# Performance work log

Hardware: AMD Instinct MI355X
Metric: run time of the kernel (lower is better)

Reference implementation:

```python
import jax, jax.numpy as jnp
import numpy as np

N_QUBITS = 12
N_LAYERS = 3
HID = 16
IN_DIM = 6
BATCH = 4096
C64 = jnp.complex64


def _ry(t):
    c = jnp.cos(t / 2).astype(C64)
    s = jnp.sin(t / 2).astype(C64)
    return jnp.stack([jnp.stack([c, -s], -1), jnp.stack([s, c], -1)], -2)


def _rx(t):
    c = jnp.cos(t / 2).astype(C64)
    s = jnp.sin(t / 2).astype(C64)
    js = 1j * s
    return jnp.stack([jnp.stack([c, -js], -1), jnp.stack([-js, c], -1)], -2)


def _rz(t):
    e = jnp.exp(-1j * t.astype(C64) / 2)
    z = jnp.zeros_like(e)
    return jnp.stack([jnp.stack([e, z], -1), jnp.stack([z, jnp.conj(e)], -1)], -2)


def _apply_1q(state, U, wire):
    # state: (B,) + (2,)*n ; U: (2,2) shared or (B,2,2) per-sample
    s = jnp.moveaxis(state, wire + 1, 1)
    if U.ndim == 2:
        s = jnp.einsum('ij,bj...->bi...', U, s)
    else:
        s = jnp.einsum('bij,bj...->bi...', U, s)
    return jnp.moveaxis(s, 1, wire + 1)


def _cnot(state, c, t):
    ax_c = c + 1
    s0 = jnp.take(state, 0, axis=ax_c)
    s1 = jnp.take(state, 1, axis=ax_c)
    t_ax = t + 1 if t < c else t  # target axis after removing control axis
    s1 = jnp.flip(s1, axis=t_ax)  # X on target when control=1
    return jnp.stack([s0, s1], axis=ax_c)


def _quantum(angles, qparams):
    # angles: (B, n_qubits) angle-encoding RY rotations; qparams: (L, n, 3)
    B = angles.shape[0]
    n = N_QUBITS
    state = jnp.zeros((B,) + (2,) * n, C64).at[(slice(None),) + (0,) * n].set(1.0)
    for i in range(n):
        state = _apply_1q(state, _ry(angles[:, i]), i)
    for l in range(N_LAYERS):
        for i in range(n):
            # RX then RY then RZ on wire i -> fused 2x2
            U = _rz(qparams[l, i, 2]) @ _ry(qparams[l, i, 1]) @ _rx(qparams[l, i, 0])
            state = _apply_1q(state, U, i)
        for i in range(n - 1):
            state = _cnot(state, i, i + 1)
        if n > 2:
            state = _cnot(state, n - 1, 0)
    p = state.real ** 2 + state.imag ** 2  # (B,) + (2,)*n
    evs = []
    for i in range(n):
        axes = tuple(a for a in range(1, n + 1) if a != i + 1)
        pi = p.sum(axes)  # (B, 2)
        evs.append(pi[:, 0] - pi[:, 1])
    return jnp.stack(evs, axis=1)  # (B, n) PauliZ expvals


def setup_inputs() -> dict:
    key = jax.random.key(0)
    ks = jax.random.split(key, 14)
    w = lambda k, shape: jax.random.normal(k, shape, jnp.float32) * 0.1
    return {
        'x': jax.random.normal(ks[0], (BATCH, IN_DIM), jnp.float32),
        'W1': w(ks[1], (HID, IN_DIM)), 'b1': w(ks[2], (HID,)),
        'W2': w(ks[3], (HID, HID)), 'b2': w(ks[4], (HID,)),
        'W3': w(ks[5], (N_QUBITS, HID)), 'b3': w(ks[6], (N_QUBITS,)),
        'qparams': w(ks[7], (N_LAYERS, N_QUBITS, 3)),
        'P1': w(ks[8], (HID, N_QUBITS)), 'c1': w(ks[9], (HID,)),
        'P2': w(ks[10], (8, HID)), 'c2': w(ks[11], (8,)),
        'P3': w(ks[12], (1, 8)), 'c3': w(ks[13], (1,)),
    }


def reference(x, W1, b1, W2, b2, W3, b3, qparams, P1, c1, P2, c2, P3, c3):
    # classical preprocessor (dropout = identity at inference)
    h = jax.nn.relu(x @ W1.T + b1)
    h = jax.nn.relu(h @ W2.T + b2)
    angles = h @ W3.T + b3  # (B, n_qubits)
    q = _quantum(angles, qparams)  # (B, n_qubits)
    # classical postprocessor
    o = jax.nn.relu(q @ P1.T + c1)
    o = jax.nn.relu(o @ P2.T + c2)
    o = jax.nn.sigmoid(o @ P3.T + c3)
    return o.squeeze(-1)  # (B,)
```

## Files before the change

kernel.cpp:

```cpp
#include <hip/hip_runtime.h>
#include <stdint.h>

#define NQ   12
#define DIM  4096
#define TPB  256

typedef float   v2f   __attribute__((ext_vector_type(2)));
typedef float   v4f   __attribute__((ext_vector_type(4)));
typedef float   f32x4 __attribute__((ext_vector_type(4)));
typedef _Float16 v2h  __attribute__((ext_vector_type(2)));
typedef _Float16 f16x8 __attribute__((ext_vector_type(8)));
typedef uint32_t u32x4 __attribute__((ext_vector_type(4)));

struct PassL {
  uint32_t v[4], m[4];
  uint32_t Be[8];
  uint8_t  np[8];
  uint8_t  layer, wb;
};
struct PassC {
  uint16_t WD[8];
  uint16_t WQ1, WQ2;
  uint16_t WV0, WV3;
  uint16_t SM[12];
  uint8_t  robin[12];
  uint8_t  layer, wb;
};
struct InitC { uint16_t ICt[8]; uint16_t ICj[16]; };

constexpr int par(uint32_t x) { return __builtin_popcount(x) & 1; }

constexpr void bmm(uint32_t* C, const uint32_t* A, const uint32_t* B) {
  for (int i = 0; i < NQ; ++i) {
    uint32_t r = 0;
    for (int j = 0; j < NQ; ++j) if ((A[i] >> j) & 1u) r ^= B[j];
    C[i] = r;
  }
}
constexpr void binv(const uint32_t* M, uint32_t* Inv) {
  uint32_t A[NQ] = {}, I[NQ] = {};
  for (int i = 0; i < NQ; ++i) { A[i] = M[i]; I[i] = 1u << i; }
  for (int c = 0; c < NQ; ++c) {
    int piv = -1;
    for (int r = c; r < NQ; ++r) if ((A[r] >> c) & 1u) { piv = r; break; }
    if (piv < 0) continue;
    uint32_t ta = A[c]; A[c] = A[piv]; A[piv] = ta;
    uint32_t ti = I[c]; I[c] = I[piv]; I[piv] = ti;
    for (int r = 0; r < NQ; ++r)
      if (r != c && ((A[r] >> c) & 1u)) { A[r] ^= A[c]; I[r] ^= I[c]; }
  }
  for (int i = 0; i < NQ; ++i) Inv[i] = I[i];
}
constexpr int rank5(const uint32_t* cols, int n) {
  uint32_t rows[5] = {}; int rnk = 0;
  for (int q = 0; q < n; ++q) {
    uint32_t x = cols[q] & 31u;
    for (int bit = 4; bit >= 0; --bit) {
      if (!((x >> bit) & 1u)) continue;
      if (rows[bit]) { x ^= rows[bit]; }
      else { rows[bit] = x; ++rnk; break; }
    }
  }
  return rnk;
}

constexpr PassL passL_default(int p) {
  PassL L{};
  uint32_t A[NQ] = {}; A[0] = 0xFFEu;
  for (int i = 1; i < NQ; ++i) A[i] = (1u << (i + 1)) - 1u;
  uint32_t A2[NQ] = {}, Ai[NQ] = {}, A2i[NQ] = {};
  bmm(A2, A, A); binv(A, Ai); binv(A2, A2i);
  const int Lr = (p < 3) ? 1 : 2, wb = (p % 3) * 4;
  const uint32_t* M  = (Lr == 1) ? A  : A2;
  const uint32_t* Mi = (Lr == 1) ? Ai : A2i;
  for (int i = 0; i < 4; ++i) {
    const int w = wb + i; uint32_t col = 0;
    for (int r = 0; r < NQ; ++r) col |= ((Mi[r] >> w) & 1u) << r;
    L.v[i] = col; L.m[i] = M[w];
  }
  uint32_t Bc[NQ] = {};
  for (int b = 0; b < NQ; ++b) {
    uint32_t col = 1u << b;
    for (int i = 0; i < 4; ++i) if ((L.m[i] >> b) & 1u) col ^= L.v[i];
    Bc[b] = col;
  }
  uint32_t redv[4] = {}; uint32_t pivmask = 0;
  for (int i = 0; i < 4; ++i) {
    redv[i] = L.v[i];
    for (int k = 0; k < i; ++k) {
      int pb = 0;
      for (int b = 0; b < NQ; ++b) if ((redv[k] >> b) & 1u) pb = b;
      if ((redv[i] >> pb) & 1u) redv[i] ^= redv[k];
    }
    int pb = 0;
    for (int b = 0; b < NQ; ++b) if ((redv[i] >> b) & 1u) pb = b;
    pivmask |= 1u << pb;
  }
  int c = 0;
  for (int b = 0; b < NQ; ++b)
    if (!((pivmask >> b) & 1u)) { L.np[c] = (uint8_t)b; L.Be[c] = Bc[b]; ++c; }
  L.layer = (uint8_t)Lr; L.wb = (uint8_t)wb;
  return L;
}

constexpr uint8_t ASSIGN[12] = {0, 1, 6, 7, 2, 3, 4, 5, 8, 9, 10, 11};
struct Lam { uint32_t minv[NQ]; };
constexpr Lam make_lam(const PassL& L) {
  uint32_t bas[12] = {L.v[0], L.v[1], L.v[2], L.v[3],
                      L.Be[0], L.Be[1], L.Be[2], L.Be[3],
                      L.Be[4], L.Be[5], L.Be[6], L.Be[7]};
  uint32_t Mr[NQ] = {};
  for (int i = 0; i < NQ; ++i) {
    uint32_t r = 0;
    for (int j = 0; j < NQ; ++j) r |= ((bas[j] >> i) & 1u) << j;
    Mr[i] = r;
  }
  Lam lm{};
  binv(Mr, lm.minv);
  return lm;
}
constexpr uint32_t lap(const Lam& lm, uint32_t y) {
  uint32_t r = 0;
  for (int j = 0; j < NQ; ++j)
    if (par(lm.minv[j] & y)) r ^= 1u << ASSIGN[j];
  return r;
}

constexpr int P4[24][4] = {
  {0,1,2,3},{0,1,3,2},{0,2,1,3},{0,2,3,1},{0,3,1,2},{0,3,2,1},
  {1,0,2,3},{1,0,3,2},{1,2,0,3},{1,2,3,0},{1,3,0,2},{1,3,2,0},
  {2,0,1,3},{2,0,3,1},{2,1,0,3},{2,1,3,0},{2,3,0,1},{2,3,1,0},
  {3,0,1,2},{3,0,2,1},{3,1,0,2},{3,1,2,0},{3,2,0,1},{3,2,1,0}};

constexpr PassL reorder_np(const PassL& L, int pi, int s45, int s67) {
  PassL T = L;
  for (int k = 0; k < 4; ++k) { T.np[k] = L.np[P4[pi][k]]; T.Be[k] = L.Be[P4[pi][k]]; }
  if (s45) { T.np[4] = L.np[5]; T.np[5] = L.np[4]; T.Be[4] = L.Be[5]; T.Be[5] = L.Be[4]; }
  if (s67) { T.np[6] = L.np[7]; T.np[7] = L.np[6]; T.Be[6] = L.Be[7]; T.Be[7] = L.Be[6]; }
  return T;
}

constexpr PassL passL_ordered(int p, const PassL& prev) {
  const PassL L = passL_default(p);
  int best = -1; PassL bestL = L;
  for (int pi = 0; pi < 24; ++pi)
  for (int s45 = 0; s45 < 2; ++s45)
  for (int s67 = 0; s67 < 2; ++s67) {
    const PassL T = reorder_np(L, pi, s45, s67);
    const Lam lm = make_lam(T);
    uint32_t g[8] = { lap(lm, prev.Be[0]), lap(lm, prev.Be[1]),
                      lap(lm, prev.Be[2]), lap(lm, prev.Be[3]),
                      lap(lm, prev.v[1]),  lap(lm, prev.v[2]),
                      lap(lm, prev.Be[6]), lap(lm, prev.Be[7]) };
    const int r = rank5(g, 8);
    if (r > best) { best = r; bestL = T; }
  }
  return bestL;
}

constexpr PassL L0 = passL_default(0);
constexpr PassL L1 = passL_ordered(1, L0);
constexpr PassL L2 = passL_ordered(2, L1);
constexpr PassL L3 = passL_ordered(3, L2);
constexpr PassL L4 = passL_ordered(4, L3);
constexpr PassL L5 = passL_ordered(5, L4);

constexpr PassC make_passC(const PassL& L, const PassL& Ln) {
  PassC c{};
  const Lam lm = make_lam(Ln);
  for (int k = 0; k < 8; ++k) c.WD[k] = (uint16_t)lap(lm, L.Be[k]);
  c.WQ1 = (uint16_t)lap(lm, L.v[1]); c.WQ2 = (uint16_t)lap(lm, L.v[2]);
  c.WV0 = (uint16_t)lap(lm, L.v[0]); c.WV3 = (uint16_t)lap(lm, L.v[3]);
  c.layer = L.layer; c.wb = L.wb;
  return c;
}
constexpr PassC make_passC5(const PassL& L) {
  PassC c{};
  uint32_t A[NQ] = {}; A[0] = 0xFFEu;
  for (int i = 1; i < NQ; ++i) A[i] = (1u << (i + 1)) - 1u;
  uint32_t A2[NQ] = {}, A3[NQ] = {};
  bmm(A2, A, A); bmm(A3, A2, A);
  for (int i = 0; i < NQ; ++i) {
    uint32_t sm = 0;
    sm |= (uint32_t)par(A3[i] & L.Be[0]) << 0;
    sm |= (uint32_t)par(A3[i] & L.Be[1]) << 1;
    sm |= (uint32_t)par(A3[i] & L.Be[2]) << 2;
    sm |= (uint32_t)par(A3[i] & L.Be[3]) << 3;
    sm |= (uint32_t)par(A3[i] & L.v[1])  << 4;
    sm |= (uint32_t)par(A3[i] & L.v[2])  << 5;
    sm |= (uint32_t)par(A3[i] & L.Be[6]) << 6;
    sm |= (uint32_t)par(A3[i] & L.Be[7]) << 7;
    c.SM[i] = (uint16_t)sm;
    uint32_t b = (uint32_t)par(A3[i] & L.v[0])
               | (uint32_t)par(A3[i] & L.v[3])  << 1
               | (uint32_t)par(A3[i] & L.Be[4]) << 2
               | (uint32_t)par(A3[i] & L.Be[5]) << 3;
    c.robin[i] = (uint8_t)b;
  }
  c.layer = L.layer; c.wb = L.wb;
  return c;
}
constexpr InitC make_init(const PassL& L) {
  InitC ic{};
  const Lam lm = make_lam(L);
  for (int b = 0; b < 8; ++b) ic.ICt[b] = (uint16_t)lap(lm, 1u << b);
  uint32_t Jc[4] = {};
  for (int b = 0; b < 4; ++b) Jc[b] = lap(lm, 1u << (8 + b));
  for (int j = 0; j < 16; ++j) {
    uint32_t r = 0;
    for (int b = 0; b < 4; ++b) if ((j >> b) & 1) r ^= Jc[b];
    ic.ICj[j] = (uint16_t)r;
  }
  return ic;
}

constexpr PassC C0 = make_passC(L0, L1);
constexpr PassC C1 = make_passC(L1, L2);
constexpr PassC C2 = make_passC(L2, L3);
constexpr PassC C3 = make_passC(L3, L4);
constexpr PassC C4 = make_passC(L4, L5);
constexpr PassC C5 = make_passC5(L5);
constexpr InitC IC = make_init(L0);

template<int P> constexpr PassC cget() {
  if constexpr (P == 0) return C0;
  else if constexpr (P == 1) return C1;
  else if constexpr (P == 2) return C2;
  else if constexpr (P == 3) return C3;
  else if constexpr (P == 4) return C4;
  else return C5;
}

__device__ __forceinline__ v2f cmulf(v2f a, v2f b) {
  return (v2f){a.x * b.x - a.y * b.y, a.x * b.y + a.y * b.x};
}
__device__ __forceinline__ uint32_t f2h2(float a, float b) {
  return __builtin_bit_cast(uint32_t, __builtin_amdgcn_cvt_pkrtz(a, b));
}
__device__ __forceinline__ uint32_t pk_rtn(float a, float b) {
  v2h h = {(_Float16)a, (_Float16)b};
  return __builtin_bit_cast(uint32_t, h);
}
__device__ __forceinline__ void build_u(const float* __restrict__ qp, int l, int w, float U[8]) {
  float p0 = qp[(l * 12 + w) * 3 + 0];
  float p1 = qp[(l * 12 + w) * 3 + 1];
  float p2 = qp[(l * 12 + w) * 3 + 2];
  float cx, sx, cy, sy, cz, sz;
  sincosf(0.5f * p0, &sx, &cx);
  sincosf(0.5f * p1, &sy, &cy);
  sincosf(0.5f * p2, &sz, &cz);
  float M00x =  cy * cx, M00y =  sy * sx;
  float M01x = -sy * cx, M01y = -cy * sx;
  float M10x =  sy * cx, M10y = -cy * sx;
  float M11x =  cy * cx, M11y = -sy * sx;
  U[0] = cz * M00x + sz * M00y; U[1] = cz * M00y - sz * M00x;
  U[2] = cz * M01x + sz * M01y; U[3] = cz * M01y - sz * M01x;
  U[4] = cz * M10x - sz * M10y; U[5] = cz * M10y + sz * M10x;
  U[6] = cz * M11x - sz * M11y; U[7] = cz * M11y + sz * M11x;
}
__device__ __forceinline__ int am_col(int c, int i) {
  return ((((c >> 2) ^ ((i >> 1) & 3)) << 2) | (c & 3));
}

template<int P>
__device__ __forceinline__ void build_am_g(uint32_t* __restrict__ Am_g,
                                           const v2f (*gg)[12][4], int t) {
  constexpr PassC pc = cget<P>();
  const int r_ = t >> 4, c_ = t & 15;
  v2f e = (v2f){1.f, 0.f};
  #pragma unroll
  for (int i = 0; i < 4; ++i) {
    v2f u = gg[pc.layer - 1][pc.wb + i][(((r_ >> i) & 1) << 1) | ((c_ >> i) & 1)];
    e = cmulf(e, u);
  }
  const int ra = 2 * r_, rb = 2 * r_ + 1;
  Am_g[P * 512 + ra * 16 + am_col(c_, ra)] = pk_rtn(e.x, -e.y);
  Am_g[P * 512 + rb * 16 + am_col(c_, rb)] = pk_rtn(e.y, e.x);
}

__global__ __launch_bounds__(256) void prep_kernel(const float* __restrict__ qp,
                                                   uint32_t* __restrict__ Am_g,
                                                   float* __restrict__ U0_g) {
  __shared__ v2f gg[2][12][4];
  const int t = threadIdx.x;
  if (t < 24) {
    const int L = t / 12 + 1, w = t % 12;
    float U[8]; build_u(qp, L, w, U);
    gg[L - 1][w][0] = (v2f){U[0], U[1]};
    gg[L - 1][w][1] = (v2f){U[2], U[3]};
    gg[L - 1][w][2] = (v2f){U[4], U[5]};
    gg[L - 1][w][3] = (v2f){U[6], U[7]};
  } else if (t >= 32 && t < 44) {
    const int w = t - 32;
    float U[8]; build_u(qp, 0, w, U);
    #pragma unroll
    for (int k = 0; k < 8; ++k) U0_g[w * 8 + k] = U[k];
  }
  __syncthreads();
  build_am_g<0>(Am_g, gg, t);
  build_am_g<1>(Am_g, gg, t);
  build_am_g<2>(Am_g, gg, t);
  build_am_g<3>(Am_g, gg, t);
  build_am_g<4>(Am_g, gg, t);
  build_am_g<5>(Am_g, gg, t);
}

template<int P, bool LAST>
__device__ __forceinline__ void do_pass(uint32_t* st, f16x8 a0, f16x8 a1,
                                        int t, float* ev) {
  constexpr PassC pc = cget<P>();
  const int lane = t & 63, wv = t >> 6;
  const int n = lane & 15, q = lane >> 4;
  const int rb = (n << 2) | (q << 6) | (wv << 10);
  int wb_ = 0;
  if constexpr (!LAST) {
    wb_ = ((n & 1) ? pc.WD[0] : 0) ^ ((n & 2) ? pc.WD[1] : 0)
        ^ ((n & 4) ? pc.WD[2] : 0) ^ ((n & 8) ? pc.WD[3] : 0)
        ^ ((q & 1) ? pc.WQ1 : 0)   ^ ((q & 2) ? pc.WQ2 : 0)
        ^ ((wv & 1) ? pc.WD[6] : 0) ^ ((wv & 2) ? pc.WD[7] : 0);
  }
  float pr[16];
  const f32x4 z = {0.f, 0.f, 0.f, 0.f};
  #pragma unroll
  for (int T = 0; T < 4; ++T) {
    u32x4 braw = *reinterpret_cast<const u32x4*>(&st[rb + (T << 8)]);
    f16x8 bf = __builtin_bit_cast(f16x8, braw);
    f32x4 c0 = __builtin_amdgcn_mfma_f32_16x16x32_f16(a0, bf, z, 0, 0, 0);
    f32x4 c1 = __builtin_amdgcn_mfma_f32_16x16x32_f16(a1, bf, z, 0, 0, 0);
    if constexpr (!LAST) {
      const int wa = wb_ ^ ((T & 1) ? pc.WD[4] : 0) ^ ((T & 2) ? pc.WD[5] : 0);
      st[wa]                       = f2h2(c0.x, c0.y);
      st[wa ^ pc.WV0]              = f2h2(c0.z, c0.w);
      st[wa ^ pc.WV3]              = f2h2(c1.x, c1.y);
      st[wa ^ (pc.WV0 ^ pc.WV3)]   = f2h2(c1.z, c1.w);
    } else {
      const int nb = ((T & 1) << 2) | ((T >> 1) << 3);
      pr[nb]     = c0.x * c0.x + c0.y * c0.y;
      pr[nb | 1] = c0.z * c0.z + c0.w * c0.w;
      pr[nb | 2] = c1.x * c1.x + c1.y * c1.y;
      pr[nb | 3] = c1.z * c1.z + c1.w * c1.w;
    }
  }
  if constexpr (LAST) {
    #pragma unroll
    for (int gs = 1; gs < 16; gs <<= 1) {
      #pragma unroll
      for (int j = 0; j < 16; ++j) {
        if (j & gs) continue;
        float u = pr[j], w2 = pr[j | gs];
        pr[j] = u + w2; pr[j | gs] = u - w2;
      }
    }
    const int pw = n | (q << 4) | (wv << 6);
    #pragma unroll
    for (int i = 0; i < NQ; ++i) {
      float h = pr[pc.robin[i]];
      int s = (__popc(pc.SM[i] & pw) & 1) << 31;
      ev[i] = __int_as_float(__float_as_int(h) ^ s);
    }
  }
}

#define LDA(P, A0, A1) {                                                        \
  const int li_ = lane & 15;                                                    \
  const int q_  = (lane >> 4) ^ ((li_ >> 1) & 3);                               \
  A0 = __builtin_bit_cast(f16x8,                                                \
      *reinterpret_cast<const u32x4*>(Am_g + (P) * 512 + li_ * 16 + q_ * 4));   \
  A1 = __builtin_bit_cast(f16x8,                                                \
      *reinterpret_cast<const u32x4*>(Am_g + (P) * 512 + (li_ + 16) * 16 + q_ * 4)); \
}

__global__ __launch_bounds__(TPB, 8) void hqc_kernel(
    const float* __restrict__ x,  const float* __restrict__ W1, const float* __restrict__ b1,
    const float* __restrict__ W2, const float* __restrict__ b2,
    const float* __restrict__ W3, const float* __restrict__ b3,
    const float* __restrict__ P1, const float* __restrict__ c1,
    const float* __restrict__ P2, const float* __restrict__ c2,
    const float* __restrict__ P3, const float* __restrict__ c3,
    const uint32_t* __restrict__ Am_g, const float* __restrict__ U0_g,
    float* __restrict__ out)
{
  __shared__ __align__(16) uint32_t st[DIM];
  __shared__ v4f  gpk0[12][2];
  __shared__ float red[4][NQ];

  const int s    = blockIdx.x;
  const int t    = threadIdx.x;
  const int lane = t & 63;
  const int wv   = t >> 6;

  f16x8 a0c, a1c, a0n, a1n;
  LDA(0, a0c, a1c)

  if (wv == 0 && lane < 16) {
    float a = b1[lane];
    #pragma unroll
    for (int k = 0; k < 6; ++k) a = fmaf(W1[lane * 6 + k], x[s * 6 + k], a);
    float h1 = fmaxf(a, 0.f);
    float a2 = b2[lane];
    #pragma unroll
    for (int k = 0; k < 16; ++k) a2 = fmaf(W2[lane * 16 + k], __shfl(h1, k, 64), a2);
    float h2 = fmaxf(a2, 0.f);
    const int lw = (lane < NQ) ? lane : 0;
    float a3 = b3[lw];
    #pragma unroll
    for (int k = 0; k < 16; ++k) a3 = fmaf(W3[lw * 16 + k], __shfl(h2, k, 64), a3);
    if (lane < NQ) {
      const float* u = U0_g + lane * 8;
      float ca, sa; sincosf(0.5f * a3, &sa, &ca);
      float c0x = u[0] * ca + u[2] * sa, c0y = u[1] * ca + u[3] * sa;
      float c1x = u[4] * ca + u[6] * sa, c1y = u[5] * ca + u[7] * sa;
      gpk0[lane][0] = (v4f){c0x, c0x, -c0y, c0y};
      gpk0[lane][1] = (v4f){c1x, c1x, -c1y, c1y};
    }
  }
  __syncthreads();

  {
    int tb = 0;
    #pragma unroll
    for (int b = 0; b < 8; ++b) if ((t >> b) & 1) tb ^= IC.ICt[b];
    v2f acc = (v2f){1.f, 0.f};
    #pragma unroll
    for (int i = 0; i < 8; ++i) {
      v4f gk = gpk0[i][(t >> i) & 1];
      acc = gk.xy * acc + gk.zw * acc.yx;
    }
    v2f l16[16];
    l16[0] = acc;
    #pragma unroll
    for (int i = 0; i < 4; ++i) {
      v4f g0 = gpk0[8 + i][0], g1 = gpk0[8 + i][1];
      #pragma unroll
      for (int j = 0; j < (1 << i); ++j) {
        v2f a = l16[j];
        l16[j | (1 << i)] = g1.xy * a + g1.zw * a.yx;
        l16[j]            = g0.xy * a + g0.zw * a.yx;
      }
    }
    #pragma unroll
    for (int j = 0; j < 16; ++j) st[tb ^ IC.ICj[j]] = f2h2(l16[j].x, l16[j].y);
  }
  __syncthreads();

  float ev[NQ];
  LDA(1, a0n, a1n)
  do_pass<0, false>(st, a0c, a1c, t, ev); __syncthreads();
  a0c = a0n; a1c = a1n; LDA(2, a0n, a1n)
  do_pass<1, false>(st, a0c, a1c, t, ev); __syncthreads();
  a0c = a0n; a1c = a1n; LDA(3, a0n, a1n)
  do_pass<2, false>(st, a0c, a1c, t, ev); __syncthreads();
  a0c = a0n; a1c = a1n; LDA(4, a0n, a1n)
  do_pass<3, false>(st, a0c, a1c, t, ev); __syncthreads();
  a0c = a0n; a1c = a1n; LDA(5, a0n, a1n)
  do_pass<4, false>(st, a0c, a1c, t, ev); __syncthreads();
  a0c = a0n; a1c = a1n;
  do_pass<5, true >(st, a0c, a1c, t, ev);

  #pragma unroll
  for (int off = 32; off >= 1; off >>= 1) {
    #pragma unroll
    for (int i = 0; i < NQ; ++i) ev[i] += __shfl_xor(ev[i], off, 64);
  }
  if (lane == 0) {
    #pragma unroll
    for (int i = 0; i < NQ; ++i) red[wv][i] = ev[i];
  }
  __syncthreads();

  if (wv == 0 && lane < 16) {
    float q = (lane < NQ)
      ? (red[0][lane] + red[1][lane] + red[2][lane] + red[3][lane])
      : 0.f;
    float a = c1[lane];
    #pragma unroll
    for (int j = 0; j < NQ; ++j) a = fmaf(P1[lane * NQ + j], __shfl(q, j, 64), a);
    float o1 = fmaxf(a, 0.f);
    float a2 = c2[lane & 7];
    #pragma unroll
    for (int j = 0; j < 16; ++j) a2 = fmaf(P2[(lane & 7) * 16 + j], __shfl(o1, j, 64), a2);
    float o2 = fmaxf(a2, 0.f);
    float a3 = c3[0];
    #pragma unroll
    for (int j = 0; j < 8; ++j) a3 = fmaf(P3[j], __shfl(o2, j, 64), a3);
    if (lane == 0) out[s] = 1.f / (1.f + expf(-a3));
  }
}

extern "C" void kernel_launch(void* const* d_in, const int* in_sizes, int n_in,
                              void* d_out, int out_size, void* d_ws, size_t ws_size,
                              hipStream_t stream) {
  (void)in_sizes; (void)n_in; (void)ws_size;
  uint32_t* Am_g = (uint32_t*)d_ws;
  float*    U0_g = (float*)((char*)d_ws + 6 * 512 * 4);
  const float* qp = (const float*)d_in[7];
  prep_kernel<<<1, 256, 0, stream>>>(qp, Am_g, U0_g);
  hqc_kernel<<<out_size, TPB, 0, stream>>>(
      (const float*)d_in[0],  (const float*)d_in[1],  (const float*)d_in[2],
      (const float*)d_in[3],  (const float*)d_in[4],  (const float*)d_in[5],
      (const float*)d_in[6],
      (const float*)d_in[8],  (const float*)d_in[9],
      (const float*)d_in[10], (const float*)d_in[11],
      (const float*)d_in[12], (const float*)d_in[13],
      Am_g, U0_g,
      (float*)d_out);
}
```

Measured before the change: 48.28 us.

## Rebuild GF(2) state basis with XOR-swizzled LDS addressing to avoid bank conflicts

Replaces the permutation-search basis selection with a new construction that picks basis vectors from neighbouring passes and solves for XOR signature corrections (G matrices). LDS read and write addresses are swizzled with these signatures so MFMA B-operand loads and fp16 writebacks land on distinct banks. When the write pattern allows it, the code emits paired adjacent stores with select-based swaps instead of four scattered stores. The cost is extra XOR address math per lane and considerably more complex compile-time construction, with some risk that the swizzle is wrong.

```diff
diff --git a/kernel.cpp b/kernel.cpp
--- a/kernel.cpp
+++ b/kernel.cpp
@@ -12,23 +12,9 @@
 typedef _Float16 f16x8 __attribute__((ext_vector_type(8)));
 typedef uint32_t u32x4 __attribute__((ext_vector_type(4)));
 
-struct PassL {
-  uint32_t v[4], m[4];
-  uint32_t Be[8];
-  uint8_t  np[8];
-  uint8_t  layer, wb;
-};
-struct PassC {
-  uint16_t WD[8];
-  uint16_t WQ1, WQ2;
-  uint16_t WV0, WV3;
-  uint16_t SM[12];
-  uint8_t  robin[12];
-  uint8_t  layer, wb;
-};
-struct InitC { uint16_t ICt[8]; uint16_t ICj[16]; };
 
 constexpr int par(uint32_t x) { return __builtin_popcount(x) & 1; }
+constexpr int chbit(uint32_t x) { int b=-1; for (int i=0;i<32;++i) if ((x>>i)&1u) b=i; return b; }
 
 constexpr void bmm(uint32_t* C, const uint32_t* A, const uint32_t* B) {
   for (int i = 0; i < NQ; ++i) {
@@ -51,185 +37,216 @@
   }
   for (int i = 0; i < NQ; ++i) Inv[i] = I[i];
 }
-constexpr int rank5(const uint32_t* cols, int n) {
-  uint32_t rows[5] = {}; int rnk = 0;
-  for (int q = 0; q < n; ++q) {
-    uint32_t x = cols[q] & 31u;
-    for (int bit = 4; bit >= 0; --bit) {
-      if (!((x >> bit) & 1u)) continue;
-      if (rows[bit]) { x ^= rows[bit]; }
-      else { rows[bit] = x; ++rnk; break; }
-    }
-  }
-  return rnk;
-}
-
-constexpr PassL passL_default(int p) {
-  PassL L{};
+
+constexpr void pass_v(int p, uint32_t* v) {
   uint32_t A[NQ] = {}; A[0] = 0xFFEu;
   for (int i = 1; i < NQ; ++i) A[i] = (1u << (i + 1)) - 1u;
   uint32_t A2[NQ] = {}, Ai[NQ] = {}, A2i[NQ] = {};
   bmm(A2, A, A); binv(A, Ai); binv(A2, A2i);
-  const int Lr = (p < 3) ? 1 : 2, wb = (p % 3) * 4;
-  const uint32_t* M  = (Lr == 1) ? A  : A2;
-  const uint32_t* Mi = (Lr == 1) ? Ai : A2i;
+  const uint32_t* Mi = (p < 3) ? Ai : A2i;
+  const int wb = (p % 3) * 4;
   for (int i = 0; i < 4; ++i) {
-    const int w = wb + i; uint32_t col = 0;
-    for (int r = 0; r < NQ; ++r) col |= ((Mi[r] >> w) & 1u) << r;
-    L.v[i] = col; L.m[i] = M[w];
-  }
-  uint32_t Bc[NQ] = {};
-  for (int b = 0; b < NQ; ++b) {
-    uint32_t col = 1u << b;
-    for (int i = 0; i < 4; ++i) if ((L.m[i] >> b) & 1u) col ^= L.v[i];
-    Bc[b] = col;
-  }
-  uint32_t redv[4] = {}; uint32_t pivmask = 0;
-  for (int i = 0; i < 4; ++i) {
-    redv[i] = L.v[i];
-    for (int k = 0; k < i; ++k) {
-      int pb = 0;
-      for (int b = 0; b < NQ; ++b) if ((redv[k] >> b) & 1u) pb = b;
-      if ((redv[i] >> pb) & 1u) redv[i] ^= redv[k];
-    }
-    int pb = 0;
-    for (int b = 0; b < NQ; ++b) if ((redv[i] >> b) & 1u) pb = b;
-    pivmask |= 1u << pb;
-  }
-  int c = 0;
-  for (int b = 0; b < NQ; ++b)
-    if (!((pivmask >> b) & 1u)) { L.np[c] = (uint8_t)b; L.Be[c] = Bc[b]; ++c; }
-  L.layer = (uint8_t)Lr; L.wb = (uint8_t)wb;
-  return L;
-}
-
-constexpr uint8_t ASSIGN[12] = {0, 1, 6, 7, 2, 3, 4, 5, 8, 9, 10, 11};
-struct Lam { uint32_t minv[NQ]; };
-constexpr Lam make_lam(const PassL& L) {
-  uint32_t bas[12] = {L.v[0], L.v[1], L.v[2], L.v[3],
-                      L.Be[0], L.Be[1], L.Be[2], L.Be[3],
-                      L.Be[4], L.Be[5], L.Be[6], L.Be[7]};
+    uint32_t col = 0;
+    for (int r = 0; r < NQ; ++r) col |= ((Mi[r] >> (wb + i)) & 1u) << r;
+    v[i] = col;
+  }
+}
+
+constexpr bool addvec(uint32_t* red, uint32_t x) {
+  while (x) {
+    const int h = chbit(x);
+    if (red[h]) x ^= red[h]; else { red[h] = x; return true; }
+  }
+  return false;
+}
+constexpr bool tryindep(const uint32_t* red, uint32_t x) {
+  uint32_t tmp[16] = {};
+  for (int i = 0; i < 16; ++i) tmp[i] = red[i];
+  return addvec(tmp, x);
+}
+
+struct B12 { uint32_t d[12]; };
+struct LC  { B12 b; uint32_t mi[12]; uint32_t G[12]; };
+
+constexpr B12 make_basis(int p) {
+  B12 b{};
+  uint32_t v[4] = {}; pass_v(p, v);
+  uint32_t red[16] = {};
+  addvec(red, v[0]); addvec(red, v[1]); addvec(red, v[2]); addvec(red, v[3]);
+  b.d[0] = v[0]; b.d[1] = v[1]; b.d[6] = v[2]; b.d[7] = v[3];
+  const int slots[8] = {2, 3, 4, 5, 8, 9, 10, 11};
+  int si = 0;
+  if (p > 0) {
+    uint32_t pv[4] = {}; pass_v(p - 1, pv);
+    if (addvec(red, pv[0])) b.d[slots[si++]] = pv[0];
+    if (addvec(red, pv[3])) b.d[slots[si++]] = pv[3];
+  }
+  for (int e = 0; e < 12 && si < 8; ++e)
+    if (addvec(red, 1u << e)) b.d[slots[si++]] = 1u << e;
+  return b;
+}
+
+constexpr uint32_t lapc(const LC& lc, uint32_t y) {
+  uint32_t r = 0;
+  for (int bb = 0; bb < 12; ++bb) r |= (uint32_t)par(lc.mi[bb] & y) << bb;
+  return r;
+}
+
+constexpr uint32_t rowbits(const uint32_t* V, int nv, int b) {
+  uint32_t r = 0;
+  for (int k = 0; k < nv; ++k) r |= ((V[k] >> b) & 1u) << k;
+  return r;
+}
+
+constexpr void solve_sig(const uint32_t* V, int nv, bool incl2, uint32_t* Cm) {
+  uint32_t red[16] = {};
+  addvec(red, rowbits(V, nv, 0));
+  addvec(red, rowbits(V, nv, 1));
+  int bs[3] = {}; int nbs = 0;
+  if (incl2) bs[nbs++] = 2;
+  bs[nbs++] = 3; bs[nbs++] = 4;
+  for (int bi = 0; bi < nbs; ++bi) {
+    const int b = bs[bi];
+    uint32_t r = rowbits(V, nv, b);
+    Cm[b] = 0;
+    if (addvec(red, r)) continue;
+    bool done = false;
+    for (int h = 5; h < 12 && !done; ++h) {
+      uint32_t cand = r ^ rowbits(V, nv, h);
+      if (tryindep(red, cand)) { addvec(red, cand); Cm[b] = 1u << h; done = true; }
+    }
+    for (int h1 = 5; h1 < 12 && !done; ++h1)
+      for (int h2 = h1 + 1; h2 < 12 && !done; ++h2) {
+        uint32_t cand = r ^ rowbits(V, nv, h1) ^ rowbits(V, nv, h2);
+        if (tryindep(red, cand)) { addvec(red, cand); Cm[b] = (1u << h1) | (1u << h2); done = true; }
+      }
+  }
+}
+
+constexpr LC make_lc(int p) {
+  LC lc{};
+  lc.b = make_basis(p);
   uint32_t Mr[NQ] = {};
   for (int i = 0; i < NQ; ++i) {
     uint32_t r = 0;
-    for (int j = 0; j < NQ; ++j) r |= ((bas[j] >> i) & 1u) << j;
+    for (int j = 0; j < NQ; ++j) r |= ((lc.b.d[j] >> i) & 1u) << j;
     Mr[i] = r;
   }
-  Lam lm{};
-  binv(Mr, lm.minv);
-  return lm;
-}
-constexpr uint32_t lap(const Lam& lm, uint32_t y) {
-  uint32_t r = 0;
-  for (int j = 0; j < NQ; ++j)
-    if (par(lm.minv[j] & y)) r ^= 1u << ASSIGN[j];
-  return r;
-}
-
-constexpr int P4[24][4] = {
-  {0,1,2,3},{0,1,3,2},{0,2,1,3},{0,2,3,1},{0,3,1,2},{0,3,2,1},
-  {1,0,2,3},{1,0,3,2},{1,2,0,3},{1,2,3,0},{1,3,0,2},{1,3,2,0},
-  {2,0,1,3},{2,0,3,1},{2,1,0,3},{2,1,3,0},{2,3,0,1},{2,3,1,0},
-  {3,0,1,2},{3,0,2,1},{3,1,0,2},{3,1,2,0},{3,2,0,1},{3,2,1,0}};
-
-constexpr PassL reorder_np(const PassL& L, int pi, int s45, int s67) {
-  PassL T = L;
-  for (int k = 0; k < 4; ++k) { T.np[k] = L.np[P4[pi][k]]; T.Be[k] = L.Be[P4[pi][k]]; }
-  if (s45) { T.np[4] = L.np[5]; T.np[5] = L.np[4]; T.Be[4] = L.Be[5]; T.Be[5] = L.Be[4]; }
-  if (s67) { T.np[6] = L.np[7]; T.np[7] = L.np[6]; T.Be[6] = L.Be[7]; T.Be[7] = L.Be[6]; }
-  return T;
-}
-
-constexpr PassL passL_ordered(int p, const PassL& prev) {
-  const PassL L = passL_default(p);
-  int best = -1; PassL bestL = L;
-  for (int pi = 0; pi < 24; ++pi)
-  for (int s45 = 0; s45 < 2; ++s45)
-  for (int s67 = 0; s67 < 2; ++s67) {
-    const PassL T = reorder_np(L, pi, s45, s67);
-    const Lam lm = make_lam(T);
-    uint32_t g[8] = { lap(lm, prev.Be[0]), lap(lm, prev.Be[1]),
-                      lap(lm, prev.Be[2]), lap(lm, prev.Be[3]),
-                      lap(lm, prev.v[1]),  lap(lm, prev.v[2]),
-                      lap(lm, prev.Be[6]), lap(lm, prev.Be[7]) };
-    const int r = rank5(g, 8);
-    if (r > best) { best = r; bestL = T; }
-  }
-  return bestL;
-}
-
-constexpr PassL L0 = passL_default(0);
-constexpr PassL L1 = passL_ordered(1, L0);
-constexpr PassL L2 = passL_ordered(2, L1);
-constexpr PassL L3 = passL_ordered(3, L2);
-constexpr PassL L4 = passL_ordered(4, L3);
-constexpr PassL L5 = passL_ordered(5, L4);
-
-constexpr PassC make_passC(const PassL& L, const PassL& Ln) {
-  PassC c{};
-  const Lam lm = make_lam(Ln);
-  for (int k = 0; k < 8; ++k) c.WD[k] = (uint16_t)lap(lm, L.Be[k]);
-  c.WQ1 = (uint16_t)lap(lm, L.v[1]); c.WQ2 = (uint16_t)lap(lm, L.v[2]);
-  c.WV0 = (uint16_t)lap(lm, L.v[0]); c.WV3 = (uint16_t)lap(lm, L.v[3]);
-  c.layer = L.layer; c.wb = L.wb;
+  binv(Mr, lc.mi);
+  uint32_t V[6] = {}; bool incl2 = false;
+  if (p == 0) {
+    for (int k = 0; k < 6; ++k) V[k] = lapc(lc, 1u << k);
+    incl2 = true;
+  } else {
+    B12 pb = make_basis(p - 1);
+    V[0] = lapc(lc, pb.d[2]); V[1] = lapc(lc, pb.d[3]);
+    V[2] = lapc(lc, pb.d[4]); V[3] = lapc(lc, pb.d[5]);
+    V[4] = lapc(lc, pb.d[1]); V[5] = lapc(lc, pb.d[6]);
+    incl2 = false;
+  }
+  uint32_t Cm[5] = {};
+  solve_sig(V, 6, incl2, Cm);
+  for (int h = 5; h < 12; ++h) {
+    uint32_t g = 0;
+    for (int b = 2; b < 5; ++b) g |= ((Cm[b] >> h) & 1u) << b;
+    lc.G[h] = g;
+  }
+  return lc;
+}
+
+constexpr uint32_t sig_of(const LC& lc, uint32_t x) {
+  uint32_t s = 0;
+  for (int h = 5; h < 12; ++h) if ((x >> h) & 1u) s ^= lc.G[h];
+  return s;
+}
+constexpr uint32_t img(const LC& lc, uint32_t y) {
+  const uint32_t l = lapc(lc, y);
+  return l ^ sig_of(lc, l);
+}
+
+struct PCon {
+  uint32_t G5, G6, G7, G10, G11;
+  uint32_t RT[4];
+  uint32_t WN[4], WQ1, WQ2, WW0, WW1, WT_[4];
+  uint32_t WV0, WV3;
+  int      W2;
+  uint32_t SM[12]; uint32_t robin[12];
+  uint8_t  layer, wb;
+};
+
+constexpr PCon make_pcon(int p) {
+  PCon c{};
+  const LC lp = make_lc(p);
+  c.G5 = lp.G[5]; c.G6 = lp.G[6]; c.G7 = lp.G[7]; c.G10 = lp.G[10]; c.G11 = lp.G[11];
+  for (int T = 0; T < 4; ++T)
+    c.RT[T] = (uint32_t)(T << 8) ^ ((T & 1) ? lp.G[8] : 0) ^ ((T & 2) ? lp.G[9] : 0);
+  c.layer = (uint8_t)((p < 3) ? 1 : 2);
+  c.wb = (uint8_t)((p % 3) * 4);
+  if (p < 5) {
+    const LC ln = make_lc(p + 1);
+    for (int k = 0; k < 4; ++k) c.WN[k] = img(ln, lp.b.d[2 + k]);
+    c.WQ1 = img(ln, lp.b.d[1]); c.WQ2 = img(ln, lp.b.d[6]);
+    c.WW0 = img(ln, lp.b.d[10]); c.WW1 = img(ln, lp.b.d[11]);
+    const uint32_t wt0 = img(ln, lp.b.d[8]), wt1 = img(ln, lp.b.d[9]);
+    for (int T = 0; T < 4; ++T) c.WT_[T] = ((T & 1) ? wt0 : 0) ^ ((T & 2) ? wt1 : 0);
+    c.WV0 = img(ln, lp.b.d[0]); c.WV3 = img(ln, lp.b.d[7]);
+    c.W2 = (c.WV0 == 4u && c.WV3 == 8u) ? 1 : 0;
+  } else {
+    uint32_t A[NQ] = {}; A[0] = 0xFFEu;
+    for (int i = 1; i < NQ; ++i) A[i] = (1u << (i + 1)) - 1u;
+    uint32_t A2[NQ] = {}, A3[NQ] = {};
+    bmm(A2, A, A); bmm(A3, A2, A);
+    for (int i = 0; i < NQ; ++i) {
+      uint32_t sm = 0;
+      sm |= (uint32_t)par(A3[i] & lp.b.d[2])  << 0;
+      sm |= (uint32_t)par(A3[i] & lp.b.d[3])  << 1;
+      sm |= (uint32_t)par(A3[i] & lp.b.d[4])  << 2;
+      sm |= (uint32_t)par(A3[i] & lp.b.d[5])  << 3;
+      sm |= (uint32_t)par(A3[i] & lp.b.d[1])  << 4;
+      sm |= (uint32_t)par(A3[i] & lp.b.d[6])  << 5;
+      sm |= (uint32_t)par(A3[i] & lp.b.d[10]) << 6;
+      sm |= (uint32_t)par(A3[i] & lp.b.d[11]) << 7;
+      c.SM[i] = sm;
+      c.robin[i] = (uint32_t)par(A3[i] & lp.b.d[0])
+                 | (uint32_t)par(A3[i] & lp.b.d[7]) << 1
+                 | (uint32_t)par(A3[i] & lp.b.d[8]) << 2
+                 | (uint32_t)par(A3[i] & lp.b.d[9]) << 3;
+    }
+  }
   return c;
 }
-constexpr PassC make_passC5(const PassL& L) {
-  PassC c{};
-  uint32_t A[NQ] = {}; A[0] = 0xFFEu;
-  for (int i = 1; i < NQ; ++i) A[i] = (1u << (i + 1)) - 1u;
-  uint32_t A2[NQ] = {}, A3[NQ] = {};
-  bmm(A2, A, A); bmm(A3, A2, A);
-  for (int i = 0; i < NQ; ++i) {
-    uint32_t sm = 0;
-    sm |= (uint32_t)par(A3[i] & L.Be[0]) << 0;
-    sm |= (uint32_t)par(A3[i] & L.Be[1]) << 1;
-    sm |= (uint32_t)par(A3[i] & L.Be[2]) << 2;
-    sm |= (uint32_t)par(A3[i] & L.Be[3]) << 3;
-    sm |= (uint32_t)par(A3[i] & L.v[1])  << 4;
-    sm |= (uint32_t)par(A3[i] & L.v[2])  << 5;
-    sm |= (uint32_t)par(A3[i] & L.Be[6]) << 6;
-    sm |= (uint32_t)par(A3[i] & L.Be[7]) << 7;
-    c.SM[i] = (uint16_t)sm;
-    uint32_t b = (uint32_t)par(A3[i] & L.v[0])
-               | (uint32_t)par(A3[i] & L.v[3])  << 1
-               | (uint32_t)par(A3[i] & L.Be[4]) << 2
-               | (uint32_t)par(A3[i] & L.Be[5]) << 3;
-    c.robin[i] = (uint8_t)b;
-  }
-  c.layer = L.layer; c.wb = L.wb;
-  return c;
-}
-constexpr InitC make_init(const PassL& L) {
+
+constexpr PCon PC0 = make_pcon(0);
+constexpr PCon PC1 = make_pcon(1);
+constexpr PCon PC2 = make_pcon(2);
+constexpr PCon PC3 = make_pcon(3);
+constexpr PCon PC4 = make_pcon(4);
+constexpr PCon PC5 = make_pcon(5);
+
+template<int P> constexpr PCon pget() {
+  if constexpr (P == 0) return PC0;
+  else if constexpr (P == 1) return PC1;
+  else if constexpr (P == 2) return PC2;
+  else if constexpr (P == 3) return PC3;
+  else if constexpr (P == 4) return PC4;
+  else return PC5;
+}
+
+struct InitC { uint32_t ICt[8]; uint32_t ICj[16]; };
+constexpr InitC make_init() {
   InitC ic{};
-  const Lam lm = make_lam(L);
-  for (int b = 0; b < 8; ++b) ic.ICt[b] = (uint16_t)lap(lm, 1u << b);
+  const LC l0 = make_lc(0);
+  for (int b = 0; b < 8; ++b) ic.ICt[b] = img(l0, 1u << b);
   uint32_t Jc[4] = {};
-  for (int b = 0; b < 4; ++b) Jc[b] = lap(lm, 1u << (8 + b));
+  for (int b = 0; b < 4; ++b) Jc[b] = img(l0, 1u << (8 + b));
   for (int j = 0; j < 16; ++j) {
     uint32_t r = 0;
     for (int b = 0; b < 4; ++b) if ((j >> b) & 1) r ^= Jc[b];
-    ic.ICj[j] = (uint16_t)r;
+    ic.ICj[j] = r;
   }
   return ic;
 }
-
-constexpr PassC C0 = make_passC(L0, L1);
-constexpr PassC C1 = make_passC(L1, L2);
-constexpr PassC C2 = make_passC(L2, L3);
-constexpr PassC C3 = make_passC(L3, L4);
-constexpr PassC C4 = make_passC(L4, L5);
-constexpr PassC C5 = make_passC5(L5);
-constexpr InitC IC = make_init(L0);
-
-template<int P> constexpr PassC cget() {
-  if constexpr (P == 0) return C0;
-  else if constexpr (P == 1) return C1;
-  else if constexpr (P == 2) return C2;
-  else if constexpr (P == 3) return C3;
-  else if constexpr (P == 4) return C4;
-  else return C5;
-}
+constexpr InitC IC = make_init();
 
 __device__ __forceinline__ v2f cmulf(v2f a, v2f b) {
   return (v2f){a.x * b.x - a.y * b.y, a.x * b.y + a.y * b.x};
@@ -265,7 +282,7 @@
 template<int P>
 __device__ __forceinline__ void build_am_g(uint32_t* __restrict__ Am_g,
                                            const v2f (*gg)[12][4], int t) {
-  constexpr PassC pc = cget<P>();
+  constexpr PCon pc = pget<P>();
   const int r_ = t >> 4, c_ = t & 15;
   v2f e = (v2f){1.f, 0.f};
   #pragma unroll
@@ -307,32 +324,45 @@
 
 template<int P, bool LAST>
 __device__ __forceinline__ void do_pass(uint32_t* st, f16x8 a0, f16x8 a1,
-                                        int t, float* ev) {
-  constexpr PassC pc = cget<P>();
-  const int lane = t & 63, wv = t >> 6;
+                                        int lane, int wvl, float* ev) {
+  constexpr PCon pc = pget<P>();
   const int n = lane & 15, q = lane >> 4;
-  const int rb = (n << 2) | (q << 6) | (wv << 10);
+  const int rb = (n << 2) ^ ((n >> 3) ? pc.G5 : 0)
+               ^ (q << 6) ^ ((q & 1) ? pc.G6 : 0) ^ ((q & 2) ? pc.G7 : 0)
+               ^ (wvl << 10) ^ ((wvl & 1) ? pc.G10 : 0) ^ ((wvl & 2) ? pc.G11 : 0);
   int wb_ = 0;
   if constexpr (!LAST) {
-    wb_ = ((n & 1) ? pc.WD[0] : 0) ^ ((n & 2) ? pc.WD[1] : 0)
-        ^ ((n & 4) ? pc.WD[2] : 0) ^ ((n & 8) ? pc.WD[3] : 0)
+    wb_ = ((n & 1) ? pc.WN[0] : 0) ^ ((n & 2) ? pc.WN[1] : 0)
+        ^ ((n & 4) ? pc.WN[2] : 0) ^ ((n & 8) ? pc.WN[3] : 0)
         ^ ((q & 1) ? pc.WQ1 : 0)   ^ ((q & 2) ? pc.WQ2 : 0)
-        ^ ((wv & 1) ? pc.WD[6] : 0) ^ ((wv & 2) ? pc.WD[7] : 0);
+        ^ ((wvl & 1) ? pc.WW0 : 0) ^ ((wvl & 2) ? pc.WW1 : 0);
   }
   float pr[16];
   const f32x4 z = {0.f, 0.f, 0.f, 0.f};
   #pragma unroll
   for (int T = 0; T < 4; ++T) {
-    u32x4 braw = *reinterpret_cast<const u32x4*>(&st[rb + (T << 8)]);
+    u32x4 braw = *reinterpret_cast<const u32x4*>(&st[rb ^ pc.RT[T]]);
     f16x8 bf = __builtin_bit_cast(f16x8, braw);
     f32x4 c0 = __builtin_amdgcn_mfma_f32_16x16x32_f16(a0, bf, z, 0, 0, 0);
     f32x4 c1 = __builtin_amdgcn_mfma_f32_16x16x32_f16(a1, bf, z, 0, 0, 0);
     if constexpr (!LAST) {
-      const int wa = wb_ ^ ((T & 1) ? pc.WD[4] : 0) ^ ((T & 2) ? pc.WD[5] : 0);
-      st[wa]                       = f2h2(c0.x, c0.y);
-      st[wa ^ pc.WV0]              = f2h2(c0.z, c0.w);
-      st[wa ^ pc.WV3]              = f2h2(c1.x, c1.y);
-      st[wa ^ (pc.WV0 ^ pc.WV3)]   = f2h2(c1.z, c1.w);
+      const int A = wb_ ^ pc.WT_[T];
+      uint32_t w00 = f2h2(c0.x, c0.y), w10 = f2h2(c0.z, c0.w);
+      uint32_t w01 = f2h2(c1.x, c1.y), w11 = f2h2(c1.z, c1.w);
+      if constexpr (pc.W2) {
+        const bool b2 = (A >> 2) & 1;
+        const int base0 = A & ~4;
+        const int base1 = base0 ^ 8;
+        st[base0]     = b2 ? w10 : w00;
+        st[base0 + 4] = b2 ? w00 : w10;
+        st[base1]     = b2 ? w11 : w01;
+        st[base1 + 4] = b2 ? w01 : w11;
+      } else {
+        st[A]                        = w00;
+        st[A ^ pc.WV0]               = w10;
+        st[A ^ pc.WV3]               = w01;
+        st[A ^ (pc.WV0 ^ pc.WV3)]    = w11;
+      }
     } else {
       const int nb = ((T & 1) << 2) | ((T >> 1) << 3);
       pr[nb]     = c0.x * c0.x + c0.y * c0.y;
@@ -351,11 +381,11 @@
         pr[j] = u + w2; pr[j | gs] = u - w2;
       }
     }
-    const int pw = n | (q << 4) | (wv << 6);
+    const int pw = n | (q << 4) | (wvl << 6);
     #pragma unroll
     for (int i = 0; i < NQ; ++i) {
       float h = pr[pc.robin[i]];
-      int s = (__popc(pc.SM[i] & pw) & 1) << 31;
+      int s = (__popc((int)pc.SM[i] & pw) & 1) << 31;
       ev[i] = __int_as_float(__float_as_int(h) ^ s);
     }
   }
@@ -445,17 +475,17 @@
 
   float ev[NQ];
   LDA(1, a0n, a1n)
-  do_pass<0, false>(st, a0c, a1c, t, ev); __syncthreads();
+  do_pass<0, false>(st, a0c, a1c, lane, wv, ev); __syncthreads();
   a0c = a0n; a1c = a1n; LDA(2, a0n, a1n)
-  do_pass<1, false>(st, a0c, a1c, t, ev); __syncthreads();
+  do_pass<1, false>(st, a0c, a1c, lane, wv, ev); __syncthreads();
   a0c = a0n; a1c = a1n; LDA(3, a0n, a1n)
-  do_pass<2, false>(st, a0c, a1c, t, ev); __syncthreads();
+  do_pass<2, false>(st, a0c, a1c, lane, wv, ev); __syncthreads();
   a0c = a0n; a1c = a1n; LDA(4, a0n, a1n)
-  do_pass<3, false>(st, a0c, a1c, t, ev); __syncthreads();
+  do_pass<3, false>(st, a0c, a1c, lane, wv, ev); __syncthreads();
   a0c = a0n; a1c = a1n; LDA(5, a0n, a1n)
-  do_pass<4, false>(st, a0c, a1c, t, ev); __syncthreads();
+  do_pass<4, false>(st, a0c, a1c, lane, wv, ev); __syncthreads();
   a0c = a0n; a1c = a1n;
-  do_pass<5, true >(st, a0c, a1c, t, ev);
+  do_pass<5, true >(st, a0c, a1c, lane, wv, ev);
 
   #pragma unroll
   for (int off = 32; off >= 1; off >>= 1) {
```

Result: slower. 58.69 us (+21.6%).
